# Kernel tuning notes

Hardware: AMD Instinct MI355X
Metric: run time of the kernel (lower is better)

The kernel has to match this reference:

```python
import jax, jax.numpy as jnp
import numpy as np

# Shapes / hyperparams (match init_kwargs and input_specs)
B, CIN, COUT, H, W = 8, 128, 128, 64, 64
K, S, P, D = 3, 1, 1, 1
KK = K * K
EPS = 1e-5  # BatchNorm eps


def setup_inputs() -> dict:
    key = jax.random.key(0)
    ks = jax.random.split(key, 4)
    x = jax.random.normal(ks[0], (B, CIN, H, W), jnp.float32)
    # small offset weights so predicted offsets stay O(1) pixels
    w_off = jax.random.normal(ks[1], (2 * KK, CIN, K, K), jnp.float32) * 0.01
    w_def = jax.random.normal(ks[2], (COUT, CIN, K, K), jnp.float32) * (1.0 / np.sqrt(CIN * KK))
    b_def = jax.random.normal(ks[3], (COUT,), jnp.float32) * 0.01
    gamma = jnp.ones((COUT,), jnp.float32)
    beta = jnp.zeros((COUT,), jnp.float32)
    return dict(x=x, w_off=w_off, w_def=w_def, b_def=b_def, gamma=gamma, beta=beta)


def _bilinear_gather(x, ys, xs):
    """x: [B,C,H,W]; ys/xs: [B,KK,Ho,Wo] float coords -> [B,C,KK,Ho,Wo].
    Zero padding outside the image (torchvision DeformConv2d semantics)."""
    Bb, C, Hh, Ww = x.shape
    y0 = jnp.floor(ys)
    x0 = jnp.floor(xs)
    wy = ys - y0
    wx = xs - x0
    xf = x.reshape(Bb, C, Hh * Ww)

    def gather(yi, xi, w):
        valid = (yi >= 0) & (yi < Hh) & (xi >= 0) & (xi < Ww)
        idx = (jnp.clip(yi, 0, Hh - 1) * Ww + jnp.clip(xi, 0, Ww - 1)).astype(jnp.int32)
        g = jnp.take_along_axis(xf, idx.reshape(Bb, 1, -1), axis=2)  # [B,C,KK*Ho*Wo]
        g = g.reshape(Bb, C, *idx.shape[1:])  # [B,C,KK,Ho,Wo]
        return g * (w * valid)[:, None]

    return (gather(y0, x0, (1 - wy) * (1 - wx))
            + gather(y0, x0 + 1, (1 - wy) * wx)
            + gather(y0 + 1, x0, wy * (1 - wx))
            + gather(y0 + 1, x0 + 1, wy * wx))


def _forward(x, w_off, w_def, b_def, gamma, beta):
    # 1) offset prediction: standard conv, no bias
    offset = jax.lax.conv_general_dilated(
        x, w_off, window_strides=(S, S), padding=((P, P), (P, P)),
        rhs_dilation=(D, D), dimension_numbers=('NCHW', 'OIHW', 'NCHW'))
    Ho, Wo = offset.shape[2], offset.shape[3]
    off = offset.reshape(B, KK, 2, Ho, Wo)  # (dy, dx) pairs per kernel loc
    dy, dx = off[:, :, 0], off[:, :, 1]

    # 2) deformable sampling coordinates
    ky = (jnp.arange(KK) // K).astype(jnp.float32) * D  # kernel row offset
    kx = (jnp.arange(KK) % K).astype(jnp.float32) * D   # kernel col offset
    base_y = (jnp.arange(Ho) * S - P).astype(jnp.float32)
    base_x = (jnp.arange(Wo) * S - P).astype(jnp.float32)
    ys = base_y[None, None, :, None] + ky[None, :, None, None] + dy  # [B,KK,Ho,Wo]
    xs = base_x[None, None, None, :] + kx[None, :, None, None] + dx

    sampled = _bilinear_gather(x, ys, xs)  # [B,CIN,KK,Ho,Wo]

    # 3) per-kernel-location weighted accumulation (implicit GEMM) + bias
    out = jnp.einsum('bckhw,ock->bohw', sampled, w_def.reshape(COUT, CIN, KK))
    out = out + b_def[None, :, None, None]

    # 4) BatchNorm2d (training mode: batch statistics) + SiLU
    mean = out.mean(axis=(0, 2, 3))
    var = out.var(axis=(0, 2, 3))
    scale = gamma / jnp.sqrt(var + EPS)
    out = (out - mean[None, :, None, None]) * scale[None, :, None, None] + beta[None, :, None, None]
    return out * jax.nn.sigmoid(out)  # SiLU


def reference(x, w_off, w_def, b_def, gamma, beta):
    return _forward(x, w_off, w_def, b_def, gamma, beta)
```

## Files before the change

### kernel.cpp

```cpp
#include <hip/hip_runtime.h>
#include <math.h>

#define CIN   128
#define COUT  128
#define KKT   9
#define NSTAT 32768.0f

typedef __attribute__((ext_vector_type(8))) short bf16x8;
typedef __attribute__((ext_vector_type(4))) float f32x4;

__device__ inline unsigned short f2bf(float f) {
    union { float f; unsigned u; } v; v.f = f;
    unsigned r = v.u + 0x7fffu + ((v.u >> 16) & 1u);
    return (unsigned short)(r >> 16);
}
__device__ inline float bflo(unsigned u) { union { unsigned u; float f; } v; v.u = u << 16; return v.f; }
__device__ inline float bfhi(unsigned u) { union { unsigned u; float f; } v; v.u = u & 0xffff0000u; return v.f; }

#define PUB_BARRIER() do { asm volatile("s_waitcnt lgkmcnt(0)" ::: "memory"); \
                           __builtin_amdgcn_s_barrier(); } while (0)


__global__ __launch_bounds__(512) void prep_all_k(const float* __restrict__ x,
                                                  unsigned* __restrict__ xt,
                                                  const float* __restrict__ w_def,
                                                  const float* __restrict__ w_off,
                                                  unsigned short* __restrict__ wb,
                                                  unsigned short* __restrict__ wob,
                                                  float* __restrict__ sums) {
    __shared__ float lt[128][65];
    const int bb = blockIdx.x;
    if (bb < 512) {
        const int b = bb >> 6, y = bb & 63;
        const int t = threadIdx.x, l = t & 63, g8 = t >> 6;
        const float* xb = x + (b * 128) * 4096 + y * 64;
#pragma unroll
        for (int pass = 0; pass < 16; pass++) {
            int c = pass * 8 + g8;
            lt[c][l] = xb[c * 4096 + l];
        }
        __syncthreads();
        unsigned* xo = xt + (bb * 64) * 64;
#pragma unroll
        for (int pass = 0; pass < 8; pass++) {
            int w = pass * 8 + g8;
            float f0 = lt[2 * l][w], f1 = lt[2 * l + 1][w];
            xo[w * 64 + l] = (unsigned)f2bf(f0) | ((unsigned)f2bf(f1) << 16);
        }
    } else {
        int i = (bb - 512) * 512 + threadIdx.x;
        if (i < 147456) {
            int oc = i / 1152, r = i - oc * 1152, kt = r >> 7, c = r & 127;
            wb[i] = f2bf(w_def[(oc * 128 + c) * 9 + kt]);
        } else if (i < 147456 + 36864) {
            int j = i - 147456;
            int ocp = j / 1152, r = j - ocp * 1152, kt = r >> 7, c = r & 127;
            wob[j] = (ocp < 18) ? f2bf(w_off[(ocp * 128 + c) * 9 + kt]) : (unsigned short)0;
        } else if (i < 147456 + 36864 + 256) {
            sums[i - 147456 - 36864] = 0.f;
        }
    }
}

#define RB 51200
__global__ __launch_bounds__(512, 4) void deform_main_k(const unsigned* __restrict__ xt,
                                                        const unsigned short* __restrict__ wb,
                                                        const unsigned short* __restrict__ wob,
                                                        const float* __restrict__ b_def,
                                                        float* __restrict__ out,
                                                        float* __restrict__ sums,
                                                        float* __restrict__ sumsq) {
    __shared__ __align__(16) unsigned char smem[RB + 4608 + 1024];
    unsigned short* xrow = (unsigned short*)smem;
    int*            tab  = (int*)smem;
    unsigned short* samp0 = (unsigned short*)(smem + 18432);
    unsigned short* samp1 = (unsigned short*)(smem + 34816);
    float* offl = (float*)(smem + RB);
    float* stat = (float*)(smem + RB + 4608);

    const int t    = threadIdx.x;
    const int bh   = blockIdx.x;
    const int b    = bh >> 6;
    const int j_   = bh & 63;
    const int h    = ((j_ & 7) << 3) | (j_ >> 3);
    const int lane = t & 63;
    const int wv   = __builtin_amdgcn_readfirstlane(t >> 6);
    const int quad = lane >> 4, lo = lane & 15;
    const int l    = lane;
    const int g    = lane >> 2;

    if (t < 256) stat[t] = 0.f;

    const unsigned* xtb = xt + b * 262144;

#pragma unroll
    for (int it = 0; it < 25; it++) {
        int p = wv + it * 8;
        if (p < 198) {
            int r = p / 66, xi = p - r * 66;
            int y = h + r - 1, x = xi - 1;
            unsigned u = 0;
            if ((unsigned)y < 64u && (unsigned)x < 64u) u = xtb[(y * 64 + x) * 64 + l];
            ((unsigned*)xrow)[(r * 66 + xi) * 64 + ((g ^ (xi & 15)) << 2) + (l & 3)] = u;
        }
    }
    __syncthreads();

    {
        const int mt = wv >> 2, nt = wv & 3;
        f32x4 ao = {0.f, 0.f, 0.f, 0.f};
        const unsigned short* wrow = wob + (mt * 16 + lo) * 1152 + quad * 8;
        for (int kt = 0; kt < 9; kt++) {
            int ky = kt / 3, kx = kt - ky * 3;
            int xi = nt * 16 + lo + kx;
#pragma unroll
            for (int ch = 0; ch < 4; ch++) {
                int gg = ch * 4 + quad;
                bf16x8 af = *(const bf16x8*)(wrow + kt * 128 + ch * 32);
                bf16x8 bf = *(const bf16x8*)(xrow + (ky * 66 + xi) * 128 + ((gg ^ (xi & 15)) << 3));
                ao = __builtin_amdgcn_mfma_f32_16x16x32_bf16(af, bf, ao, 0, 0, 0);
            }
        }
        __syncthreads();
#pragma unroll
        for (int r = 0; r < 4; r++) {
            int oc = mt * 16 + quad * 4 + r;
            if (oc < 18) offl[oc * 64 + nt * 16 + lo] = ao[r];
        }
    }
    __syncthreads();

    for (int i = t; i < KKT * 64; i += 512) {
        int k = i >> 6, w2 = i & 63;
        float dy = offl[(2 * k) * 64 + w2];
        float dx = offl[(2 * k + 1) * 64 + w2];
        int ky = k / 3, kx = k - ky * 3;
        float ys = (float)(h - 1 + ky) + dy;
        float xs = (float)(w2 - 1 + kx) + dx;
        float y0f = floorf(ys), x0f = floorf(xs);
        float wyf = ys - y0f, wxf = xs - x0f;
        int iy0 = (int)y0f, ix0 = (int)x0f;
        int cy0 = min(max(iy0, 0), 63), cy1 = min(max(iy0 + 1, 0), 63);
        int px  = min(max(ix0, 0), 63), px2 = min(max(ix0 + 1, 0), 63);
        float wy0 = (iy0 >= 0 && iy0 < 64) ? (1.f - wyf) : 0.f;
        float wy1 = (iy0 + 1 >= 0 && iy0 + 1 < 64) ? wyf : 0.f;
        float wa  = (ix0 >= 0 && ix0 < 64) ? (1.f - wxf) : 0.f;
        float wbv = (ix0 + 1 >= 0 && ix0 + 1 < 64) ? wxf : 0.f;
        int base = i * 8;
        tab[base + 0] = (cy0 * 64 + px ) * 64;
        tab[base + 1] = (cy0 * 64 + px2) * 64;
        tab[base + 2] = (cy1 * 64 + px ) * 64;
        tab[base + 3] = (cy1 * 64 + px2) * 64;
        ((float*)tab)[base + 4] = wy0 * wa;
        ((float*)tab)[base + 5] = wy0 * wbv;
        ((float*)tab)[base + 6] = wy1 * wa;
        ((float*)tab)[base + 7] = wy1 * wbv;
    }
    __syncthreads();

    const int m0 = wv >> 1, n0 = wv & 1;
    const int w0 = wv * 8;
    f32x4 acc[2][2];
#pragma unroll
    for (int i = 0; i < 2; i++)
#pragma unroll
        for (int j = 0; j < 2; j++)
#pragma unroll
            for (int r = 0; r < 4; r++) acc[i][j][r] = 0.f;

    const unsigned short* wrow0 = wb + (2 * m0 * 16 + lo) * 1152 + quad * 8;
    const unsigned short* wrow1 = wrow0 + 16 * 1152;

    unsigned u0[8], u1[8], u2[8], u3[8];

#pragma unroll
    for (int i = 0; i < 8; i++) {
        const int4 a = *(const int4*)&tab[(w0 + i) * 8];
        u0[i] = xtb[a.x + l]; u1[i] = xtb[a.y + l];
        u2[i] = xtb[a.z + l]; u3[i] = xtb[a.w + l];
    }

    for (int kt = 0; kt < KKT; kt++) {
        unsigned* sb = (unsigned*)((kt & 1) ? samp1 : samp0);
#pragma unroll
        for (int i = 0; i < 8; i++) {
            const float4 tw = *(const float4*)&tab[(kt * 64 + w0 + i) * 8 + 4];
            float e = tw.x * bflo(u0[i]);
            e = fmaf(tw.y, bflo(u1[i]), e);
            e = fmaf(tw.z, bflo(u2[i]), e);
            e = fmaf(tw.w, bflo(u3[i]), e);
            float o = tw.x * bfhi(u0[i]);
            o = fmaf(tw.y, bfhi(u1[i]), o);
            o = fmaf(tw.z, bfhi(u2[i]), o);
            o = fmaf(tw.w, bfhi(u3[i]), o);
            unsigned pk;
            asm("v_cvt_pk_bf16_f32 %0, %1, %2" : "=v"(pk) : "v"(e), "v"(o));
            int w = w0 + i;
            sb[w * 64 + ((g ^ (w & 15)) << 2) + (l & 3)] = pk;
        }
        bf16x8 af0[4], af1[4];
#pragma unroll
        for (int ch = 0; ch < 4; ch++) {
            af0[ch] = *(const bf16x8*)(wrow0 + kt * 128 + ch * 32);
            af1[ch] = *(const bf16x8*)(wrow1 + kt * 128 + ch * 32);
        }
        if (kt < KKT - 1) {
#pragma unroll
            for (int i = 0; i < 8; i++) {
                const int4 a = *(const int4*)&tab[((kt + 1) * 64 + w0 + i) * 8];
                u0[i] = xtb[a.x + l]; u1[i] = xtb[a.y + l];
                u2[i] = xtb[a.z + l]; u3[i] = xtb[a.w + l];
            }
        }
        PUB_BARRIER();
        const unsigned short* sbs = (kt & 1) ? samp1 : samp0;
#pragma unroll
        for (int ch = 0; ch < 4; ch++) {
            int gg = ch * 4 + quad;
            int r0 = (2 * n0 + 0) * 16 + lo, r1 = (2 * n0 + 1) * 16 + lo;
            bf16x8 bf0 = *(const bf16x8*)(sbs + r0 * 128 + ((gg ^ lo) << 3));
            bf16x8 bf1 = *(const bf16x8*)(sbs + r1 * 128 + ((gg ^ lo) << 3));
            acc[0][0] = __builtin_amdgcn_mfma_f32_16x16x32_bf16(af0[ch], bf0, acc[0][0], 0, 0, 0);
            acc[0][1] = __builtin_amdgcn_mfma_f32_16x16x32_bf16(af0[ch], bf1, acc[0][1], 0, 0, 0);
            acc[1][0] = __builtin_amdgcn_mfma_f32_16x16x32_bf16(af1[ch], bf0, acc[1][0], 0, 0, 0);
            acc[1][1] = __builtin_amdgcn_mfma_f32_16x16x32_bf16(af1[ch], bf1, acc[1][1], 0, 0, 0);
        }
    }

    float* ob = out + b * COUT * 4096 + h * 64;
#pragma unroll
    for (int mt2 = 0; mt2 < 2; mt2++) {
        int ocb = (2 * m0 + mt2) * 16 + quad * 4;
#pragma unroll
        for (int r = 0; r < 4; r++) {
            int oc = ocb + r;
            float bia = b_def[oc];
            float ssum = 0.f, qsum = 0.f;
#pragma unroll
            for (int nt2 = 0; nt2 < 2; nt2++) {
                int w_ = (2 * n0 + nt2) * 16 + lo;
                float v = acc[mt2][nt2][r] + bia;
                ob[oc * 4096 + w_] = v;
                ssum += v; qsum += v * v;
            }
#pragma unroll
            for (int d = 1; d < 16; d <<= 1) {
                ssum += __shfl_xor(ssum, d, 64);
                qsum += __shfl_xor(qsum, d, 64);
            }
            if (lo == 0) { atomicAdd(&stat[oc], ssum); atomicAdd(&stat[128 + oc], qsum); }
        }
    }
    __syncthreads();
    if (t < 256) {
        float* gp = (t < 128) ? (sums + t) : (sumsq + (t - 128));
        atomicAdd(gp, stat[t]);
    }
}

__global__ __launch_bounds__(256) void bn_silu_k(float* __restrict__ out,
                                                 const float* __restrict__ sums,
                                                 const float* __restrict__ sumsq,
                                                 const float* __restrict__ gamma,
                                                 const float* __restrict__ beta) {
    __shared__ float sc_s[128], sh_s[128];
    int t = threadIdx.x;
    if (t < 128) {
        const float invN = 1.f / NSTAT;
        float m = sums[t] * invN;
        float v = fmaf(-m, m, sumsq[t] * invN);
        float sc = gamma[t] * rsqrtf(v + 1e-5f);
        sc_s[t] = sc;
        sh_s[t] = beta[t] - m * sc;
    }
    __syncthreads();
    int i = blockIdx.x * 256 + t;
    float4 v = ((float4*)out)[i];
    int oc = (i >> 10) & 127;
    float sc = sc_s[oc], sh = sh_s[oc];
    float z0 = v.x * sc + sh;
    float z1 = v.y * sc + sh;
    float z2 = v.z * sc + sh;
    float z3 = v.w * sc + sh;
    v.x = z0 / (1.f + __expf(-z0));
    v.y = z1 / (1.f + __expf(-z1));
    v.z = z2 / (1.f + __expf(-z2));
    v.w = z3 / (1.f + __expf(-z3));
    ((float4*)out)[i] = v;
}

extern "C" void kernel_launch(void* const* d_in, const int* in_sizes, int n_in,
                              void* d_out, int out_size, void* d_ws, size_t ws_size,
                              hipStream_t stream) {
    const float* x     = (const float*)d_in[0];
    const float* w_off = (const float*)d_in[1];
    const float* w_def = (const float*)d_in[2];
    const float* b_def = (const float*)d_in[3];
    const float* gamma = (const float*)d_in[4];
    const float* beta  = (const float*)d_in[5];
    float* out = (float*)d_out;

    unsigned*       xt   = (unsigned*)d_ws;
    unsigned short* wb   = (unsigned short*)((char*)d_ws + 16777216);
    unsigned short* wob  = (unsigned short*)((char*)d_ws + 17072128);
    float*          sums = (float*)((char*)d_ws + 17145856);
    float*          sumsq = sums + 128;

    prep_all_k<<<873, 512, 0, stream>>>(x, xt, w_def, w_off, wb, wob, sums);
    deform_main_k<<<512, 512, 0, stream>>>(xt, wb, wob, b_def, out, sums, sumsq);
    bn_silu_k<<<4096, 256, 0, stream>>>(out, sums, sumsq, gamma, beta);
}
```

Measured before the change: 158.2 us.

## Double deform kernel block to 1024 threads and split MFMA tiles per wave

Raises the deformable-conv block from 8 to 16 waves. Each wave now gathers 4 output columns instead of 8 and computes one 16-row output-channel tile across two column tiles, down from a 2x2 tile grid. It also overlaps the offset buffer with the sample buffer to shrink LDS and uses packed float2 math for the bilinear blend. The aim is more latency hiding for the irregular global gathers, at the cost of more A-operand (weight) reloads per wave and higher register and barrier pressure.

```diff
diff --git a/kernel.cpp b/kernel.cpp
--- a/kernel.cpp
+++ b/kernel.cpp
@@ -8,14 +8,18 @@
 
 typedef __attribute__((ext_vector_type(8))) short bf16x8;
 typedef __attribute__((ext_vector_type(4))) float f32x4;
+typedef __attribute__((ext_vector_type(2))) float f32x2;
 
 __device__ inline unsigned short f2bf(float f) {
     union { float f; unsigned u; } v; v.f = f;
     unsigned r = v.u + 0x7fffu + ((v.u >> 16) & 1u);
     return (unsigned short)(r >> 16);
 }
-__device__ inline float bflo(unsigned u) { union { unsigned u; float f; } v; v.u = u << 16; return v.f; }
-__device__ inline float bfhi(unsigned u) { union { unsigned u; float f; } v; v.u = u & 0xffff0000u; return v.f; }
+__device__ inline f32x2 bf2(unsigned u) {
+    union { unsigned u; float f; } lo, hi;
+    lo.u = u << 16; hi.u = u & 0xffff0000u;
+    f32x2 r; r[0] = lo.f; r[1] = hi.f; return r;
+}
 
 #define PUB_BARRIER() do { asm volatile("s_waitcnt lgkmcnt(0)" ::: "memory"); \
                            __builtin_amdgcn_s_barrier(); } while (0)
@@ -62,21 +66,20 @@
     }
 }
 
-#define RB 51200
-__global__ __launch_bounds__(512, 4) void deform_main_k(const unsigned* __restrict__ xt,
-                                                        const unsigned short* __restrict__ wb,
-                                                        const unsigned short* __restrict__ wob,
-                                                        const float* __restrict__ b_def,
-                                                        float* __restrict__ out,
-                                                        float* __restrict__ sums,
-                                                        float* __restrict__ sumsq) {
-    __shared__ __align__(16) unsigned char smem[RB + 4608 + 1024];
-    unsigned short* xrow = (unsigned short*)smem;
-    int*            tab  = (int*)smem;
+__global__ __launch_bounds__(1024, 8) void deform_main_k(const unsigned* __restrict__ xt,
+                                                         const unsigned short* __restrict__ wb,
+                                                         const unsigned short* __restrict__ wob,
+                                                         const float* __restrict__ b_def,
+                                                         float* __restrict__ out,
+                                                         float* __restrict__ sums,
+                                                         float* __restrict__ sumsq) {
+    __shared__ __align__(16) unsigned char smem[52224];
+    unsigned short* xrow  = (unsigned short*)smem;
+    int*            tab   = (int*)smem;
     unsigned short* samp0 = (unsigned short*)(smem + 18432);
     unsigned short* samp1 = (unsigned short*)(smem + 34816);
-    float* offl = (float*)(smem + RB);
-    float* stat = (float*)(smem + RB + 4608);
+    float* offl = (float*)(smem + 34816);
+    float* stat = (float*)(smem + 51200);
 
     const int t    = threadIdx.x;
     const int bh   = blockIdx.x;
@@ -89,13 +92,11 @@
     const int l    = lane;
     const int g    = lane >> 2;
 
-    if (t < 256) stat[t] = 0.f;
-
     const unsigned* xtb = xt + b * 262144;
 
 #pragma unroll
-    for (int it = 0; it < 25; it++) {
-        int p = wv + it * 8;
+    for (int it = 0; it < 13; it++) {
+        int p = wv + it * 16;
         if (p < 198) {
             int r = p / 66, xi = p - r * 66;
             int y = h + r - 1, x = xi - 1;
@@ -106,13 +107,13 @@
     }
     __syncthreads();
 
-    {
-        const int mt = wv >> 2, nt = wv & 3;
-        f32x4 ao = {0.f, 0.f, 0.f, 0.f};
-        const unsigned short* wrow = wob + (mt * 16 + lo) * 1152 + quad * 8;
+    const int omt = wv >> 2, ont = wv & 3;
+    f32x4 ao = {0.f, 0.f, 0.f, 0.f};
+    if (wv < 8) {
+        const unsigned short* wrow = wob + (omt * 16 + lo) * 1152 + quad * 8;
         for (int kt = 0; kt < 9; kt++) {
             int ky = kt / 3, kx = kt - ky * 3;
-            int xi = nt * 16 + lo + kx;
+            int xi = ont * 16 + lo + kx;
 #pragma unroll
             for (int ch = 0; ch < 4; ch++) {
                 int gg = ch * 4 + quad;
@@ -121,16 +122,18 @@
                 ao = __builtin_amdgcn_mfma_f32_16x16x32_bf16(af, bf, ao, 0, 0, 0);
             }
         }
-        __syncthreads();
+    }
+    __syncthreads();
+    if (wv < 8) {
 #pragma unroll
         for (int r = 0; r < 4; r++) {
-            int oc = mt * 16 + quad * 4 + r;
-            if (oc < 18) offl[oc * 64 + nt * 16 + lo] = ao[r];
-        }
-    }
-    __syncthreads();
-
-    for (int i = t; i < KKT * 64; i += 512) {
+            int oc = omt * 16 + quad * 4 + r;
+            if (oc < 18) offl[oc * 64 + ont * 16 + lo] = ao[r];
+        }
+    }
+    __syncthreads();
+
+    for (int i = t; i < KKT * 64; i += 1024) {
         int k = i >> 6, w2 = i & 63;
         float dy = offl[(2 * k) * 64 + w2];
         float dx = offl[(2 * k + 1) * 64 + w2];
@@ -156,26 +159,24 @@
         ((float*)tab)[base + 6] = wy1 * wa;
         ((float*)tab)[base + 7] = wy1 * wbv;
     }
-    __syncthreads();
-
-    const int m0 = wv >> 1, n0 = wv & 1;
-    const int w0 = wv * 8;
-    f32x4 acc[2][2];
-#pragma unroll
-    for (int i = 0; i < 2; i++)
-#pragma unroll
-        for (int j = 0; j < 2; j++)
-#pragma unroll
-            for (int r = 0; r < 4; r++) acc[i][j][r] = 0.f;
-
-    const unsigned short* wrow0 = wb + (2 * m0 * 16 + lo) * 1152 + quad * 8;
-    const unsigned short* wrow1 = wrow0 + 16 * 1152;
-
-    unsigned u0[8], u1[8], u2[8], u3[8];
-
-#pragma unroll
-    for (int i = 0; i < 8; i++) {
-        const int4 a = *(const int4*)&tab[(w0 + i) * 8];
+    if (t < 256) stat[t] = 0.f;
+    __syncthreads();
+
+    const int ot  = wv & 7;
+    const int ph  = wv >> 3;
+    const int w0p = wv * 4;
+    f32x4 acc[2];
+#pragma unroll
+    for (int j = 0; j < 2; j++)
+#pragma unroll
+        for (int r = 0; r < 4; r++) acc[j][r] = 0.f;
+
+    const unsigned short* wrow = wb + (ot * 16 + lo) * 1152 + quad * 8;
+
+    unsigned u0[4], u1[4], u2[4], u3[4];
+#pragma unroll
+    for (int i = 0; i < 4; i++) {
+        const int4 a = *(const int4*)&tab[(w0p + i) * 8];
         u0[i] = xtb[a.x + l]; u1[i] = xtb[a.y + l];
         u2[i] = xtb[a.z + l]; u3[i] = xtb[a.w + l];
     }
@@ -183,31 +184,21 @@
     for (int kt = 0; kt < KKT; kt++) {
         unsigned* sb = (unsigned*)((kt & 1) ? samp1 : samp0);
 #pragma unroll
-        for (int i = 0; i < 8; i++) {
-            const float4 tw = *(const float4*)&tab[(kt * 64 + w0 + i) * 8 + 4];
-            float e = tw.x * bflo(u0[i]);
-            e = fmaf(tw.y, bflo(u1[i]), e);
-            e = fmaf(tw.z, bflo(u2[i]), e);
-            e = fmaf(tw.w, bflo(u3[i]), e);
-            float o = tw.x * bfhi(u0[i]);
-            o = fmaf(tw.y, bfhi(u1[i]), o);
-            o = fmaf(tw.z, bfhi(u2[i]), o);
-            o = fmaf(tw.w, bfhi(u3[i]), o);
+        for (int i = 0; i < 4; i++) {
+            const float4 tw = *(const float4*)&tab[(kt * 64 + w0p + i) * 8 + 4];
+            f32x2 s = bf2(u0[i]) * tw.x;
+            s += bf2(u1[i]) * tw.y;
+            s += bf2(u2[i]) * tw.z;
+            s += bf2(u3[i]) * tw.w;
             unsigned pk;
-            asm("v_cvt_pk_bf16_f32 %0, %1, %2" : "=v"(pk) : "v"(e), "v"(o));
-            int w = w0 + i;
+            asm("v_cvt_pk_bf16_f32 %0, %1, %2" : "=v"(pk) : "v"(s[0]), "v"(s[1]));
+            int w = w0p + i;
             sb[w * 64 + ((g ^ (w & 15)) << 2) + (l & 3)] = pk;
         }
-        bf16x8 af0[4], af1[4];
-#pragma unroll
-        for (int ch = 0; ch < 4; ch++) {
-            af0[ch] = *(const bf16x8*)(wrow0 + kt * 128 + ch * 32);
-            af1[ch] = *(const bf16x8*)(wrow1 + kt * 128 + ch * 32);
-        }
         if (kt < KKT - 1) {
 #pragma unroll
-            for (int i = 0; i < 8; i++) {
-                const int4 a = *(const int4*)&tab[((kt + 1) * 64 + w0 + i) * 8];
+            for (int i = 0; i < 4; i++) {
+                const int4 a = *(const int4*)&tab[((kt + 1) * 64 + w0p + i) * 8];
                 u0[i] = xtb[a.x + l]; u1[i] = xtb[a.y + l];
                 u2[i] = xtb[a.z + l]; u3[i] = xtb[a.w + l];
             }
@@ -216,40 +207,36 @@
         const unsigned short* sbs = (kt & 1) ? samp1 : samp0;
 #pragma unroll
         for (int ch = 0; ch < 4; ch++) {
+            bf16x8 af = *(const bf16x8*)(wrow + kt * 128 + ch * 32);
             int gg = ch * 4 + quad;
-            int r0 = (2 * n0 + 0) * 16 + lo, r1 = (2 * n0 + 1) * 16 + lo;
-            bf16x8 bf0 = *(const bf16x8*)(sbs + r0 * 128 + ((gg ^ lo) << 3));
-            bf16x8 bf1 = *(const bf16x8*)(sbs + r1 * 128 + ((gg ^ lo) << 3));
-            acc[0][0] = __builtin_amdgcn_mfma_f32_16x16x32_bf16(af0[ch], bf0, acc[0][0], 0, 0, 0);
-            acc[0][1] = __builtin_amdgcn_mfma_f32_16x16x32_bf16(af0[ch], bf1, acc[0][1], 0, 0, 0);
-            acc[1][0] = __builtin_amdgcn_mfma_f32_16x16x32_bf16(af1[ch], bf0, acc[1][0], 0, 0, 0);
-            acc[1][1] = __builtin_amdgcn_mfma_f32_16x16x32_bf16(af1[ch], bf1, acc[1][1], 0, 0, 0);
+#pragma unroll
+            for (int jj = 0; jj < 2; jj++) {
+                int j = 2 * ph + jj;
+                bf16x8 bfv = *(const bf16x8*)(sbs + (j * 16 + lo) * 128 + ((gg ^ lo) << 3));
+                acc[jj] = __builtin_amdgcn_mfma_f32_16x16x32_bf16(af, bfv, acc[jj], 0, 0, 0);
+            }
         }
     }
 
     float* ob = out + b * COUT * 4096 + h * 64;
 #pragma unroll
-    for (int mt2 = 0; mt2 < 2; mt2++) {
-        int ocb = (2 * m0 + mt2) * 16 + quad * 4;
-#pragma unroll
-        for (int r = 0; r < 4; r++) {
-            int oc = ocb + r;
-            float bia = b_def[oc];
-            float ssum = 0.f, qsum = 0.f;
-#pragma unroll
-            for (int nt2 = 0; nt2 < 2; nt2++) {
-                int w_ = (2 * n0 + nt2) * 16 + lo;
-                float v = acc[mt2][nt2][r] + bia;
-                ob[oc * 4096 + w_] = v;
-                ssum += v; qsum += v * v;
-            }
-#pragma unroll
-            for (int d = 1; d < 16; d <<= 1) {
-                ssum += __shfl_xor(ssum, d, 64);
-                qsum += __shfl_xor(qsum, d, 64);
-            }
-            if (lo == 0) { atomicAdd(&stat[oc], ssum); atomicAdd(&stat[128 + oc], qsum); }
-        }
+    for (int r = 0; r < 4; r++) {
+        int oc = ot * 16 + quad * 4 + r;
+        float bia = b_def[oc];
+        float ssum = 0.f, qsum = 0.f;
+#pragma unroll
+        for (int jj = 0; jj < 2; jj++) {
+            int j = 2 * ph + jj;
+            float v = acc[jj][r] + bia;
+            ob[oc * 4096 + j * 16 + lo] = v;
+            ssum += v; qsum += v * v;
+        }
+#pragma unroll
+        for (int d = 1; d < 16; d <<= 1) {
+            ssum += __shfl_xor(ssum, d, 64);
+            qsum += __shfl_xor(qsum, d, 64);
+        }
+        if (lo == 0) { atomicAdd(&stat[oc], ssum); atomicAdd(&stat[128 + oc], qsum); }
     }
     __syncthreads();
     if (t < 256) {
@@ -307,6 +294,6 @@
     float*          sumsq = sums + 128;
 
     prep_all_k<<<873, 512, 0, stream>>>(x, xt, w_def, w_off, wb, wob, sums);
-    deform_main_k<<<512, 512, 0, stream>>>(xt, wb, wob, b_def, out, sums, sumsq);
+    deform_main_k<<<512, 1024, 0, stream>>>(xt, wb, wob, b_def, out, sums, sumsq);
     bn_silu_k<<<4096, 256, 0, stream>>>(out, sums, sumsq, gamma, beta);
 }
```

New measurement: 153.6 us. 2.9% less time.
